# Kernel tuning notes

Hardware: AMD Instinct MI355X
Metric: run time of the kernel (lower is better)

Reference implementation:

```python
import jax, jax.numpy as jnp
import numpy as np

B, T, C = 8, 1024, 1024   # batch, seq (== block_size), n_embed
H, D = 16, 64             # num_heads, head_size


def setup_inputs() -> dict:
    key = jax.random.key(0)
    kx, kq, kk, kv = jax.random.split(key, 4)
    scale = C ** -0.5  # mimic nn.Linear init scale roughly
    return {
        "x": jax.random.normal(kx, (B, T, C), dtype=jnp.float32),
        "Wq": jax.random.normal(kq, (H, C, D), dtype=jnp.float32) * scale,
        "Wk": jax.random.normal(kk, (H, C, D), dtype=jnp.float32) * scale,
        "Wv": jax.random.normal(kv, (H, C, D), dtype=jnp.float32) * scale,
    }


def reference(x, Wq, Wk, Wv):
    # Per-head Q/K/V projections (batched over heads instead of a Python loop)
    q = jnp.einsum("btc,hcd->bhtd", x, Wq)
    k = jnp.einsum("btc,hcd->bhtd", x, Wk)
    v = jnp.einsum("btc,hcd->bhtd", x, Wv)

    # scaled causal attention scores: [B, H, T, T]
    scores = jnp.einsum("bhtd,bhsd->bhts", q, k) * (D ** -0.5)
    causal = jnp.tril(jnp.ones((T, T), dtype=bool))
    scores = jnp.where(causal, scores, jnp.finfo(scores.dtype).min)
    attn = jax.nn.softmax(scores, axis=-1)

    out = jnp.einsum("bhts,bhsd->bhtd", attn, v)  # [B, H, T, D]
    # concat heads along last dim -> [B, T, H*D]
    return out.transpose(0, 2, 1, 3).reshape(B, T, H * D)
```

## Files before the change

kernel.cpp:

```cpp
#include <hip/hip_runtime.h>
#include <hip/hip_bf16.h>
#include <cstdint>


typedef __attribute__((ext_vector_type(8))) short short8;
typedef __attribute__((ext_vector_type(4))) short bfs4;
typedef __attribute__((ext_vector_type(4))) float f32x4;
typedef __attribute__((ext_vector_type(4))) int   i32x4;

__device__ __forceinline__ unsigned short f2bf(float f) {
  union { float f; unsigned int u; } v; v.f = f;
  unsigned int u = v.u;
  return (unsigned short)((u + 0x7fffu + ((u >> 16) & 1u)) >> 16);
}

__device__ __forceinline__ unsigned int pk_bf16(float a, float b) {
  union { __hip_bfloat162 h; unsigned int u; } cv;
  cv.h = __float22bfloat162_rn(make_float2(a, b));
  return cv.u;
}

__global__ __launch_bounds__(256) void k_convert_x(const float* __restrict__ x,
                                                   unsigned short* __restrict__ xb) {
  int g = blockIdx.x * 256 + threadIdx.x;
  const float4* xp = (const float4*)x + (size_t)g * 2;
  float4 a = xp[0], b = xp[1];
  short8 o;
  o[0] = (short)f2bf(a.x); o[1] = (short)f2bf(a.y);
  o[2] = (short)f2bf(a.z); o[3] = (short)f2bf(a.w);
  o[4] = (short)f2bf(b.x); o[5] = (short)f2bf(b.y);
  o[6] = (short)f2bf(b.z); o[7] = (short)f2bf(b.w);
  *(short8*)(xb + (size_t)g * 8) = o;
}

__global__ __launch_bounds__(256) void k_convert_w(const float* __restrict__ Wq,
                                                   const float* __restrict__ Wk,
                                                   const float* __restrict__ Wv,
                                                   unsigned short* __restrict__ Wt) {
  int g = blockIdx.x * 256 + threadIdx.x;
  int d  = g & 63;
  int cb = (g >> 6) & 127;
  int h  = (g >> 13) & 15;
  int p  = g >> 17;
  const float* W = (p == 0) ? Wq : (p == 1) ? Wk : Wv;
  const float* src = W + ((size_t)h * 1024 + cb * 8) * 64 + d;
  short8 o;
#pragma unroll
  for (int j = 0; j < 8; ++j) o[j] = (short)f2bf(src[(size_t)j * 64]);
  *(short8*)(Wt + (((size_t)p * 16 + h) * 64 + d) * 1024 + cb * 8) = o;
}

__global__ __launch_bounds__(256) void k_proj(const unsigned short* __restrict__ xb,
                                              const unsigned short* __restrict__ Wt,
                                              unsigned short* __restrict__ Qb,
                                              unsigned short* __restrict__ Kb,
                                              unsigned short* __restrict__ Vt) {
  __shared__ alignas(16) unsigned short As[8192];
  __shared__ alignas(16) unsigned short Bs[8192];
  const int p   = blockIdx.y;
  const int bx  = blockIdx.x;
  const int tid = threadIdx.x;
  const int lane = tid & 63, w = tid >> 6;
  const int ln = lane & 15, quad = lane >> 4;
  const int wm = w >> 1, wn = w & 1;

  const unsigned short* Abase;
  const unsigned short* Bbase;
  int m0, n0;
  const int c = bx & 7, j = bx >> 3;
  if (p < 2) {
    Abase = xb; Bbase = Wt + (size_t)p * 1048576;
    m0 = ((j >> 3) * 8 + c) * 128;
    n0 = (j & 7) * 128;
  } else {
    Abase = Wt + (size_t)2 * 1048576; Bbase = xb;
    n0 = ((j >> 3) * 8 + c) * 128;
    m0 = (j & 7) * 128;
  }

  i32x4 ra[4], rb[4];
  auto ld = [&](int kt) {
    const int c0 = kt * 64;
#pragma unroll
    for (int i = 0; i < 4; ++i) {
      int idx = i * 256 + tid;
      int iln = idx & 15, iq = (idx >> 4) & 3, imt = (idx >> 6) & 7, ikk = (idx >> 9) & 1;
      int row = imt * 16 + iln;
      int col = c0 + ikk * 32 + iq * 8;
      ra[i] = *(const i32x4*)(Abase + (size_t)(m0 + row) * 1024 + col);
      rb[i] = *(const i32x4*)(Bbase + (size_t)(n0 + row) * 1024 + col);
    }
  };

  f32x4 acc[4][4];
#pragma unroll
  for (int i = 0; i < 4; ++i)
#pragma unroll
    for (int jj = 0; jj < 4; ++jj) acc[i][jj] = (f32x4){0.f, 0.f, 0.f, 0.f};

  ld(0);
  for (int kt = 0; kt < 16; ++kt) {
#pragma unroll
    for (int i = 0; i < 4; ++i) {
      *(i32x4*)((char*)As + (size_t)(i * 256 + tid) * 16) = ra[i];
      *(i32x4*)((char*)Bs + (size_t)(i * 256 + tid) * 16) = rb[i];
    }
    __syncthreads();
    if (kt < 15) ld(kt + 1);

#pragma unroll
    for (int kk = 0; kk < 2; ++kk) {
      short8 af[4], bfr[4];
#pragma unroll
      for (int t4 = 0; t4 < 4; ++t4) {
        af[t4]  = *(const short8*)&As[(size_t)((((kk * 8 + wm * 4 + t4) * 4 + quad) * 16 + ln)) * 8];
        bfr[t4] = *(const short8*)&Bs[(size_t)((((kk * 8 + wn * 4 + t4) * 4 + quad) * 16 + ln)) * 8];
      }
#pragma unroll
      for (int mt = 0; mt < 4; ++mt)
#pragma unroll
        for (int nt = 0; nt < 4; ++nt)
          acc[mt][nt] = __builtin_amdgcn_mfma_f32_16x16x32_bf16(
              af[mt], bfr[nt], acc[mt][nt], 0, 0, 0);
    }
    __syncthreads();
  }

  unsigned short* outp = (p == 0) ? Qb : (p == 1) ? Kb : Vt;
#pragma unroll
  for (int mt = 0; mt < 4; ++mt)
#pragma unroll
    for (int nt = 0; nt < 4; ++nt)
#pragma unroll
      for (int r = 0; r < 4; ++r) {
        int m = m0 + (wm * 4 + mt) * 16 + quad * 4 + r;
        int n = n0 + (wn * 4 + nt) * 16 + ln;
        size_t addr;
        if (p < 2) {
          addr = ((size_t)(m >> 10) * 16 + (n >> 6)) * 65536 + (size_t)(m & 1023) * 64 + (n & 63);
        } else {
          addr = ((size_t)(n >> 10) * 1024 + m) * 1024 + (n & 1023);
        }
        outp[addr] = f2bf(acc[mt][nt][r]);
      }
}

__global__ __launch_bounds__(256) void k_attn(const unsigned short* __restrict__ Qb,
                                              const unsigned short* __restrict__ Kb,
                                              const unsigned short* __restrict__ Vt,
                                              float* __restrict__ out) {
  __shared__ alignas(16) unsigned short Ks[4096];
  __shared__ alignas(16) unsigned short Vs[4096];
  __shared__ alignas(16) unsigned short Ps[8192];
  const int bid = blockIdx.x;
  const int qb = 7 - (bid >> 7);
  const int bh = bid & 127;
  const int b = bh >> 4, h = bh & 15;
  const int tid = threadIdx.x, lane = tid & 63, w = tid >> 6;
  const int ln = lane & 15, quad = lane >> 4;

  i32x4 rk[2], rv[2];
  auto ldkv = [&](int kt) {
    const int s0 = kt * 64;
#pragma unroll
    for (int i = 0; i < 2; ++i) {
      int idx = i * 256 + tid;
      int iln = idx & 15, iq = (idx >> 4) & 3, ikk = (idx >> 6) & 1, it = (idx >> 7) & 3;
      rk[i] = *(const i32x4*)(Kb + ((size_t)bh * 1024 + s0 + it * 16 + iln) * 64 + ikk * 32 + iq * 8);
      rv[i] = *(const i32x4*)(Vt + ((size_t)bh * 64 + it * 16 + iln) * 1024 + s0 + ikk * 32 + iq * 8);
    }
  };

  short8 qf[2][2];
#pragma unroll
  for (int qt = 0; qt < 2; ++qt) {
    const int q = qb * 128 + qt * 64 + w * 16 + ln;
#pragma unroll
    for (int kk = 0; kk < 2; ++kk)
      qf[qt][kk] = *(const short8*)(Qb + ((size_t)bh * 1024 + q) * 64 + kk * 32 + quad * 8);
  }

  f32x4 o[2][4];
#pragma unroll
  for (int qt = 0; qt < 2; ++qt)
#pragma unroll
    for (int dt = 0; dt < 4; ++dt) o[qt][dt] = (f32x4){0.f, 0.f, 0.f, 0.f};
  float l_i[2] = {0.f, 0.f};
  const float sc = 0.18033688011112042f;
  const float FM = 16.0f;

  const int ktmax = 2 * qb + 1;
  ldkv(0);

  for (int kt = 0; kt <= ktmax; ++kt) {
    const int s0 = kt * 64;
#pragma unroll
    for (int i = 0; i < 2; ++i) {
      *(i32x4*)((char*)Ks + (size_t)(i * 256 + tid) * 16) = rk[i];
      *(i32x4*)((char*)Vs + (size_t)(i * 256 + tid) * 16) = rv[i];
    }
    __syncthreads();
    if (kt < ktmax) ldkv(kt + 1);

    f32x4 st[2][4];
#pragma unroll
    for (int s = 0; s < 4; ++s) {
      st[0][s] = (f32x4){0.f, 0.f, 0.f, 0.f};
      st[1][s] = (f32x4){0.f, 0.f, 0.f, 0.f};
#pragma unroll
      for (int kk = 0; kk < 2; ++kk) {
        short8 kf = *(const short8*)&Ks[(size_t)(((s * 2 + kk) * 4 + quad) * 16 + ln) * 8];
        st[0][s] = __builtin_amdgcn_mfma_f32_16x16x32_bf16(kf, qf[0][kk], st[0][s], 0, 0, 0);
        st[1][s] = __builtin_amdgcn_mfma_f32_16x16x32_bf16(kf, qf[1][kk], st[1][s], 0, 0, 0);
      }
    }

#pragma unroll
    for (int qt = 0; qt < 2; ++qt) {
      const int q = qb * 128 + qt * 64 + w * 16 + ln;
      const bool masked = (kt >= 2 * qb + qt);
      float pv[4][4];
      float rs = 0.f;
#pragma unroll
      for (int s = 0; s < 4; ++s)
#pragma unroll
        for (int r = 0; r < 4; ++r) {
          float v = fmaf(st[qt][s][r], sc, -FM);
          if (masked) {
            int sidx = s0 + s * 16 + quad * 4 + r;
            if (sidx > q) v = -1.0e30f;
          }
          float e = __builtin_amdgcn_exp2f(v);
          pv[s][r] = e;
          rs += e;
        }
      rs += __shfl_xor(rs, 16);
      rs += __shfl_xor(rs, 32);
      l_i[qt] += rs;

      unsigned short* Pq = Ps + (w * 2 + qt) * 1024;
#pragma unroll
      for (int s = 0; s < 4; ++s) {
        union { bfs4 v; unsigned int u[2]; } pk;
        pk.u[0] = pk_bf16(pv[s][0], pv[s][1]);
        pk.u[1] = pk_bf16(pv[s][2], pv[s][3]);
        *(bfs4*)&Pq[(s * 2 + (quad >> 1)) * 128 + ln * 8 + (quad & 1) * 4] = pk.v;
      }
    }

#pragma unroll
    for (int kk = 0; kk < 2; ++kk) {
      short8 pf0 = *(const short8*)&Ps[(size_t)(w * 2 + 0) * 1024 + (size_t)((kk * 4 + quad) * 16 + ln) * 8];
      short8 pf1 = *(const short8*)&Ps[(size_t)(w * 2 + 1) * 1024 + (size_t)((kk * 4 + quad) * 16 + ln) * 8];
#pragma unroll
      for (int dt = 0; dt < 4; ++dt) {
        short8 vf = *(const short8*)&Vs[(size_t)(((dt * 2 + kk) * 4 + quad) * 16 + ln) * 8];
        o[0][dt] = __builtin_amdgcn_mfma_f32_16x16x32_bf16(vf, pf0, o[0][dt], 0, 0, 0);
        o[1][dt] = __builtin_amdgcn_mfma_f32_16x16x32_bf16(vf, pf1, o[1][dt], 0, 0, 0);
      }
    }

    __syncthreads();
  }

#pragma unroll
  for (int qt = 0; qt < 2; ++qt) {
    const int q = qb * 128 + qt * 64 + w * 16 + ln;
    const float rl = 1.0f / l_i[qt];
#pragma unroll
    for (int dt = 0; dt < 4; ++dt) {
      float4 ov;
      ov.x = o[qt][dt][0] * rl; ov.y = o[qt][dt][1] * rl;
      ov.z = o[qt][dt][2] * rl; ov.w = o[qt][dt][3] * rl;
      *(float4*)(out + ((size_t)b * 1024 + q) * 1024 + h * 64 + dt * 16 + quad * 4) = ov;
    }
  }
}

extern "C" void kernel_launch(void* const* d_in, const int* in_sizes, int n_in,
                              void* d_out, int out_size, void* d_ws, size_t ws_size,
                              hipStream_t stream) {
  const float* x  = (const float*)d_in[0];
  const float* Wq = (const float*)d_in[1];
  const float* Wk = (const float*)d_in[2];
  const float* Wv = (const float*)d_in[3];
  float* out = (float*)d_out;

  unsigned short* ws = (unsigned short*)d_ws;
  unsigned short* xb = ws;
  unsigned short* Wt = ws + 8388608;
  unsigned short* Qb = ws + 11534336;
  unsigned short* Kb = ws + 19922944;
  unsigned short* Vt = ws + 28311552;

  hipLaunchKernelGGL(k_convert_x, dim3(4096), dim3(256), 0, stream, x, xb);
  hipLaunchKernelGGL(k_convert_w, dim3(1536), dim3(256), 0, stream, Wq, Wk, Wv, Wt);
  hipLaunchKernelGGL(k_proj, dim3(512, 3), dim3(256), 0, stream, xb, Wt, Qb, Kb, Vt);
  hipLaunchKernelGGL(k_attn, dim3(1024), dim3(256), 0, stream, Qb, Kb, Vt, out);
}
```

Measured before the change: 232.1 us.

## Halve attention query tile and load K/V directly into LDS

Each attention block now handles 64 queries instead of 128, so the grid doubles to 2048 blocks and per-block state shrinks (P buffer halved, one set of accumulators). The register-staged K/V prefetch is replaced by global_load_lds direct-to-LDS copies followed by a full waitcnt and barrier. This aims to improve load balance and occupancy on the causal triangle and to cut register pressure and LDS store instructions. In exchange, the software overlap of the next tile's load with compute is lost, and K/V are re-read twice as often across blocks.

New measurement: 233.0 us. No clear change (+0.4%).

```diff
diff --git a/kernel.cpp b/kernel.cpp
--- a/kernel.cpp
+++ b/kernel.cpp
@@ -7,6 +7,13 @@
 typedef __attribute__((ext_vector_type(4))) short bfs4;
 typedef __attribute__((ext_vector_type(4))) float f32x4;
 typedef __attribute__((ext_vector_type(4))) int   i32x4;
+
+typedef const __attribute__((address_space(1))) void* gas1_t;
+typedef __attribute__((address_space(3))) void* las3_t;
+
+__device__ __forceinline__ void gl_lds16(const void* g, void* l) {
+  __builtin_amdgcn_global_load_lds((gas1_t)g, (las3_t)l, 16, 0, 0);
+}
 
 __device__ __forceinline__ unsigned short f2bf(float f) {
   union { float f; unsigned int u; } v; v.f = f;
@@ -151,129 +158,100 @@
                                               float* __restrict__ out) {
   __shared__ alignas(16) unsigned short Ks[4096];
   __shared__ alignas(16) unsigned short Vs[4096];
-  __shared__ alignas(16) unsigned short Ps[8192];
+  __shared__ alignas(16) unsigned short Ps[4096];
   const int bid = blockIdx.x;
-  const int qb = 7 - (bid >> 7);
+  const int qb = 15 - (bid >> 7);
   const int bh = bid & 127;
   const int b = bh >> 4, h = bh & 15;
   const int tid = threadIdx.x, lane = tid & 63, w = tid >> 6;
   const int ln = lane & 15, quad = lane >> 4;
-
-  i32x4 rk[2], rv[2];
-  auto ldkv = [&](int kt) {
+  const int q = qb * 64 + w * 16 + ln;
+
+  short8 qf[2];
+#pragma unroll
+  for (int kk = 0; kk < 2; ++kk)
+    qf[kk] = *(const short8*)(Qb + ((size_t)bh * 1024 + q) * 64 + kk * 32 + quad * 8);
+
+  f32x4 o[4];
+#pragma unroll
+  for (int dt = 0; dt < 4; ++dt) o[dt] = (f32x4){0.f, 0.f, 0.f, 0.f};
+  float l_i = 0.f;
+  const float sc = 0.18033688011112042f;
+  const float FM = 16.0f;
+
+  for (int kt = 0; kt <= qb; ++kt) {
     const int s0 = kt * 64;
+    __syncthreads();
 #pragma unroll
     for (int i = 0; i < 2; ++i) {
       int idx = i * 256 + tid;
       int iln = idx & 15, iq = (idx >> 4) & 3, ikk = (idx >> 6) & 1, it = (idx >> 7) & 3;
-      rk[i] = *(const i32x4*)(Kb + ((size_t)bh * 1024 + s0 + it * 16 + iln) * 64 + ikk * 32 + iq * 8);
-      rv[i] = *(const i32x4*)(Vt + ((size_t)bh * 64 + it * 16 + iln) * 1024 + s0 + ikk * 32 + iq * 8);
-    }
-  };
-
-  short8 qf[2][2];
-#pragma unroll
-  for (int qt = 0; qt < 2; ++qt) {
-    const int q = qb * 128 + qt * 64 + w * 16 + ln;
-#pragma unroll
-    for (int kk = 0; kk < 2; ++kk)
-      qf[qt][kk] = *(const short8*)(Qb + ((size_t)bh * 1024 + q) * 64 + kk * 32 + quad * 8);
-  }
-
-  f32x4 o[2][4];
-#pragma unroll
-  for (int qt = 0; qt < 2; ++qt)
-#pragma unroll
-    for (int dt = 0; dt < 4; ++dt) o[qt][dt] = (f32x4){0.f, 0.f, 0.f, 0.f};
-  float l_i[2] = {0.f, 0.f};
-  const float sc = 0.18033688011112042f;
-  const float FM = 16.0f;
-
-  const int ktmax = 2 * qb + 1;
-  ldkv(0);
-
-  for (int kt = 0; kt <= ktmax; ++kt) {
-    const int s0 = kt * 64;
-#pragma unroll
-    for (int i = 0; i < 2; ++i) {
-      *(i32x4*)((char*)Ks + (size_t)(i * 256 + tid) * 16) = rk[i];
-      *(i32x4*)((char*)Vs + (size_t)(i * 256 + tid) * 16) = rv[i];
-    }
-    __syncthreads();
-    if (kt < ktmax) ldkv(kt + 1);
-
-    f32x4 st[2][4];
+      char* lk = (char*)Ks + (size_t)(i * 256 + (tid & ~63)) * 16;
+      char* lv = (char*)Vs + (size_t)(i * 256 + (tid & ~63)) * 16;
+      gl_lds16(Kb + ((size_t)bh * 1024 + s0 + it * 16 + iln) * 64 + ikk * 32 + iq * 8, lk);
+      gl_lds16(Vt + ((size_t)bh * 64 + it * 16 + iln) * 1024 + s0 + ikk * 32 + iq * 8, lv);
+    }
+    __builtin_amdgcn_s_waitcnt(0);
+    __syncthreads();
+
+    f32x4 st[4];
 #pragma unroll
     for (int s = 0; s < 4; ++s) {
-      st[0][s] = (f32x4){0.f, 0.f, 0.f, 0.f};
-      st[1][s] = (f32x4){0.f, 0.f, 0.f, 0.f};
+      st[s] = (f32x4){0.f, 0.f, 0.f, 0.f};
 #pragma unroll
       for (int kk = 0; kk < 2; ++kk) {
         short8 kf = *(const short8*)&Ks[(size_t)(((s * 2 + kk) * 4 + quad) * 16 + ln) * 8];
-        st[0][s] = __builtin_amdgcn_mfma_f32_16x16x32_bf16(kf, qf[0][kk], st[0][s], 0, 0, 0);
-        st[1][s] = __builtin_amdgcn_mfma_f32_16x16x32_bf16(kf, qf[1][kk], st[1][s], 0, 0, 0);
-      }
-    }
-
-#pragma unroll
-    for (int qt = 0; qt < 2; ++qt) {
-      const int q = qb * 128 + qt * 64 + w * 16 + ln;
-      const bool masked = (kt >= 2 * qb + qt);
-      float pv[4][4];
-      float rs = 0.f;
-#pragma unroll
-      for (int s = 0; s < 4; ++s)
-#pragma unroll
-        for (int r = 0; r < 4; ++r) {
-          float v = fmaf(st[qt][s][r], sc, -FM);
-          if (masked) {
-            int sidx = s0 + s * 16 + quad * 4 + r;
-            if (sidx > q) v = -1.0e30f;
-          }
-          float e = __builtin_amdgcn_exp2f(v);
-          pv[s][r] = e;
-          rs += e;
+        st[s] = __builtin_amdgcn_mfma_f32_16x16x32_bf16(kf, qf[kk], st[s], 0, 0, 0);
+      }
+    }
+
+    const bool diag = (kt == qb);
+    float pv[4][4];
+    float rs = 0.f;
+#pragma unroll
+    for (int s = 0; s < 4; ++s)
+#pragma unroll
+      for (int r = 0; r < 4; ++r) {
+        float v = fmaf(st[s][r], sc, -FM);
+        if (diag) {
+          int sidx = s0 + s * 16 + quad * 4 + r;
+          if (sidx > q) v = -1.0e30f;
         }
-      rs += __shfl_xor(rs, 16);
-      rs += __shfl_xor(rs, 32);
-      l_i[qt] += rs;
-
-      unsigned short* Pq = Ps + (w * 2 + qt) * 1024;
-#pragma unroll
-      for (int s = 0; s < 4; ++s) {
-        union { bfs4 v; unsigned int u[2]; } pk;
-        pk.u[0] = pk_bf16(pv[s][0], pv[s][1]);
-        pk.u[1] = pk_bf16(pv[s][2], pv[s][3]);
-        *(bfs4*)&Pq[(s * 2 + (quad >> 1)) * 128 + ln * 8 + (quad & 1) * 4] = pk.v;
-      }
+        float e = __builtin_amdgcn_exp2f(v);
+        pv[s][r] = e;
+        rs += e;
+      }
+    rs += __shfl_xor(rs, 16);
+    rs += __shfl_xor(rs, 32);
+    l_i += rs;
+
+    unsigned short* Pq = Ps + w * 1024;
+#pragma unroll
+    for (int s = 0; s < 4; ++s) {
+      union { bfs4 v; unsigned int u[2]; } pk;
+      pk.u[0] = pk_bf16(pv[s][0], pv[s][1]);
+      pk.u[1] = pk_bf16(pv[s][2], pv[s][3]);
+      *(bfs4*)&Pq[(s * 2 + (quad >> 1)) * 128 + ln * 8 + (quad & 1) * 4] = pk.v;
     }
 
 #pragma unroll
     for (int kk = 0; kk < 2; ++kk) {
-      short8 pf0 = *(const short8*)&Ps[(size_t)(w * 2 + 0) * 1024 + (size_t)((kk * 4 + quad) * 16 + ln) * 8];
-      short8 pf1 = *(const short8*)&Ps[(size_t)(w * 2 + 1) * 1024 + (size_t)((kk * 4 + quad) * 16 + ln) * 8];
+      short8 pf = *(const short8*)&Pq[(size_t)((kk * 4 + quad) * 16 + ln) * 8];
 #pragma unroll
       for (int dt = 0; dt < 4; ++dt) {
         short8 vf = *(const short8*)&Vs[(size_t)(((dt * 2 + kk) * 4 + quad) * 16 + ln) * 8];
-        o[0][dt] = __builtin_amdgcn_mfma_f32_16x16x32_bf16(vf, pf0, o[0][dt], 0, 0, 0);
-        o[1][dt] = __builtin_amdgcn_mfma_f32_16x16x32_bf16(vf, pf1, o[1][dt], 0, 0, 0);
-      }
-    }
-
-    __syncthreads();
-  }
-
-#pragma unroll
-  for (int qt = 0; qt < 2; ++qt) {
-    const int q = qb * 128 + qt * 64 + w * 16 + ln;
-    const float rl = 1.0f / l_i[qt];
-#pragma unroll
-    for (int dt = 0; dt < 4; ++dt) {
-      float4 ov;
-      ov.x = o[qt][dt][0] * rl; ov.y = o[qt][dt][1] * rl;
-      ov.z = o[qt][dt][2] * rl; ov.w = o[qt][dt][3] * rl;
-      *(float4*)(out + ((size_t)b * 1024 + q) * 1024 + h * 64 + dt * 16 + quad * 4) = ov;
-    }
+        o[dt] = __builtin_amdgcn_mfma_f32_16x16x32_bf16(vf, pf, o[dt], 0, 0, 0);
+      }
+    }
+  }
+
+  const float rl = 1.0f / l_i;
+#pragma unroll
+  for (int dt = 0; dt < 4; ++dt) {
+    float4 ov;
+    ov.x = o[dt][0] * rl; ov.y = o[dt][1] * rl;
+    ov.z = o[dt][2] * rl; ov.w = o[dt][3] * rl;
+    *(float4*)(out + ((size_t)b * 1024 + q) * 1024 + h * 64 + dt * 16 + quad * 4) = ov;
   }
 }
 
@@ -296,5 +274,5 @@
   hipLaunchKernelGGL(k_convert_x, dim3(4096), dim3(256), 0, stream, x, xb);
   hipLaunchKernelGGL(k_convert_w, dim3(1536), dim3(256), 0, stream, Wq, Wk, Wv, Wt);
   hipLaunchKernelGGL(k_proj, dim3(512, 3), dim3(256), 0, stream, xb, Wt, Qb, Kb, Vt);
-  hipLaunchKernelGGL(k_attn, dim3(1024), dim3(256), 0, stream, Qb, Kb, Vt, out);
-}
+  hipLaunchKernelGGL(k_attn, dim3(2048), dim3(256), 0, stream, Qb, Kb, Vt, out);
+}
```
